# Performance work log

Hardware: AMD Instinct MI355X
Metric: run time of the kernel (lower is better)

The kernel has to match this reference:

```python
import jax, jax.numpy as jnp
import numpy as np

B, S, D, H, HD, FFN_MULT = 4, 2048, 2048, 16, 128, 4
EPS = 1e-8


def setup_inputs() -> dict:
    key = jax.random.key(0)
    ks = jax.random.split(key, 12)
    s = lambda k, shape, scale: (jax.random.normal(k, shape, dtype=jnp.float32) * scale)
    d_ff = D * FFN_MULT
    return {
        "x": s(ks[0], (B, S, D), 1.0),
        # per-head Q/K/V projections, stacked: [H, D, HD] (no bias, as in source)
        "wq": s(ks[1], (H, D, HD), D ** -0.5),
        "wk": s(ks[2], (H, D, HD), D ** -0.5),
        "wv": s(ks[3], (H, D, HD), D ** -0.5),
        # output projection Linear(D, D) with bias
        "wo": s(ks[4], (D, D), D ** -0.5),
        "bo": jnp.zeros((D,), jnp.float32),
        # FFN: Linear(D, d_ff) -> ReLU -> Linear(d_ff, D), both with bias
        "w1": s(ks[5], (D, d_ff), D ** -0.5),
        "b1": jnp.zeros((d_ff,), jnp.float32),
        "w2": s(ks[6], (d_ff, D), d_ff ** -0.5),
        "b2": jnp.zeros((D,), jnp.float32),
        # RMSNorm gains
        "g1": jnp.ones((D,), jnp.float32),
        "g2": jnp.ones((D,), jnp.float32),
    }


def rms_norm(x, g):
    return x * jax.lax.rsqrt(jnp.mean(x * x, axis=-1, keepdims=True) + EPS) * g


def attention(h, wq, wk, wv, wo, bo):
    # per-head projections batched over heads: [B,S,D] x [H,D,K] -> [B,H,S,K]
    q = jnp.einsum("bsd,hdk->bhsk", h, wq)
    k = jnp.einsum("bsd,hdk->bhsk", h, wk)
    v = jnp.einsum("bsd,hdk->bhsk", h, wv)
    scores = jnp.einsum("bhsk,bhtk->bhst", q, k) * (HD ** -0.5)
    causal = jnp.tril(jnp.ones((S, S), dtype=bool))
    scores = jnp.where(causal, scores, -jnp.inf)
    attn = jax.nn.softmax(scores, axis=-1)
    out = jnp.einsum("bhst,bhtk->bhsk", attn, v)  # [B,H,S,HD]
    # concat heads along feature dim (head order matches torch.cat over heads)
    out = out.transpose(0, 2, 1, 3).reshape(B, S, D)
    return out @ wo + bo


def reference(x, wq, wk, wv, wo, bo, w1, b1, w2, b2, g1, g2):
    x = x + attention(rms_norm(x, g1), wq, wk, wv, wo, bo)
    h = rms_norm(x, g2)
    ffn = jax.nn.relu(h @ w1 + b1) @ w2 + b2
    return x + ffn
```

## Files before the change

kernel.cpp:

```cpp
#include <hip/hip_runtime.h>
#include <hip/hip_bf16.h>

#define Bsz 4
#define Ssz 2048
#define Dsz 2048
#define Hn 16
#define HDsz 128
#define DFF 8192
#define Msz (Bsz*Ssz)

typedef __bf16 bf16x8 __attribute__((ext_vector_type(8)));
typedef float  f32x4  __attribute__((ext_vector_type(4)));

enum { FLAG_BIAS=1, FLAG_RELU=2, FLAG_RESID=4, FLAG_F32OUT=8 };

#define GLDS16(g, l) __builtin_amdgcn_global_load_lds( \
    (const __attribute__((address_space(1))) unsigned int*)(g), \
    (__attribute__((address_space(3))) unsigned int*)(l), 16, 0, 0)

template <typename TIN>
__global__ __launch_bounds__(256) void transpose_cvt(
    const TIN* __restrict__ in, __bf16* __restrict__ out,
    int R, int C, long long inRS, int subB,
    long long strideOuter, long long strideInner, long long outBS)
{
  __shared__ float tile[32][33];
  int bz = blockIdx.z;
  const TIN* inp = in + (size_t)(bz / subB) * strideOuter + (size_t)(bz % subB) * strideInner;
  __bf16* outp = out + (size_t)bz * outBS;
  int tx = threadIdx.x, ty = threadIdx.y;
  int c  = blockIdx.x * 32 + tx;
  int r0 = blockIdx.y * 32;
#pragma unroll
  for (int i = 0; i < 4; ++i) {
    int r = r0 + ty + i * 8;
    tile[ty + i * 8][tx] = (float)inp[(size_t)r * inRS + c];
  }
  __syncthreads();
  int oc  = r0 + tx;
  int or0 = blockIdx.x * 32;
#pragma unroll
  for (int i = 0; i < 4; ++i) {
    int orr = or0 + ty + i * 8;
    outp[(size_t)orr * R + oc] = (__bf16)tile[tx][ty + i * 8];
  }
}

__global__ __launch_bounds__(256) void rmsnorm_k(
    const float* __restrict__ x, const float* __restrict__ g, __bf16* __restrict__ out)
{
  int row = blockIdx.x, tid = threadIdx.x;
  const float4* xr = (const float4*)(x + (size_t)row * Dsz);
  float4 v0 = xr[tid*2], v1 = xr[tid*2+1];
  float ss = v0.x*v0.x + v0.y*v0.y + v0.z*v0.z + v0.w*v0.w
           + v1.x*v1.x + v1.y*v1.y + v1.z*v1.z + v1.w*v1.w;
#pragma unroll
  for (int off = 32; off > 0; off >>= 1) ss += __shfl_down(ss, off);
  __shared__ float wsum[4];
  __shared__ float sc;
  if ((tid & 63) == 0) wsum[tid >> 6] = ss;
  __syncthreads();
  if (tid == 0) {
    float t = wsum[0] + wsum[1] + wsum[2] + wsum[3];
    sc = rsqrtf(t * (1.0f / (float)Dsz) + 1e-8f);
  }
  __syncthreads();
  float s = sc;
  const float4* gr = (const float4*)g;
  float4 g0 = gr[tid*2], g1v = gr[tid*2+1];
  bf16x8 ov;
  ov[0]=(__bf16)(v0.x*s*g0.x);  ov[1]=(__bf16)(v0.y*s*g0.y);
  ov[2]=(__bf16)(v0.z*s*g0.z);  ov[3]=(__bf16)(v0.w*s*g0.w);
  ov[4]=(__bf16)(v1.x*s*g1v.x); ov[5]=(__bf16)(v1.y*s*g1v.y);
  ov[6]=(__bf16)(v1.z*s*g1v.z); ov[7]=(__bf16)(v1.w*s*g1v.w);
  *(bf16x8*)(out + (size_t)row * Dsz + tid * 8) = ov;
}

#define SBAR       asm volatile("s_barrier" ::: "memory")
#define WAIT_LGKM0 do { asm volatile("s_waitcnt lgkmcnt(0)" ::: "memory"); \
                        __builtin_amdgcn_sched_barrier(0); } while(0)
#define WAIT_VM4   asm volatile("s_waitcnt vmcnt(4)" ::: "memory")
#define WAIT_VM0   asm volatile("s_waitcnt vmcnt(0)" ::: "memory")

#define STAGE(Xb, Xlds, nb, kh, kst) do { \
    GLDS16((Xb) + (size_t)(rloc      ) * K + (kst) + (kh)*32 + sloc, (Xlds) + (nb)*32768 + (kh)*16384 +        wuni); \
    GLDS16((Xb) + (size_t)(rloc + 128) * K + (kst) + (kh)*32 + sloc, (Xlds) + (nb)*32768 + (kh)*16384 + 8192 + wuni); \
  } while (0)

#define LDA(mh, kh, i) (*(const bf16x8*)(AsB + cur*32768 + (kh)*16384 + (wr*128 + (mh)*64 + (i)*16 + l15)*64 + psl))
#define LDB(kh, j)     (*(const bf16x8*)(BsB + cur*32768 + (kh)*16384 + (wc*64  + (j)*16 + l15)*64 + psl))

#define MFMA16(mh) do { \
  _Pragma("unroll") \
  for (int mi = 0; mi < 4; ++mi) \
    _Pragma("unroll") \
    for (int nj = 0; nj < 4; ++nj) \
      acc[(mh)*4+mi][nj] = __builtin_amdgcn_mfma_f32_16x16x32_bf16(af[mi], bf[nj], acc[(mh)*4+mi][nj], 0, 0, 0); \
} while (0)

__global__ __launch_bounds__(512) void gemm256(
    const __bf16* __restrict__ A, const __bf16* __restrict__ B,
    const float* __restrict__ bias, const float* __restrict__ resid,
    void* __restrict__ Cout, int M, int N, int K, int flags)
{
  __shared__ __align__(16) __bf16 As[2*2*256*32];
  __shared__ __align__(16) __bf16 Bs[2*2*256*32];
  int nwg = gridDim.x;
  int id = blockIdx.x;
  id = (id & 7) * (nwg >> 3) + (id >> 3);
  int ntn = N >> 8;
  int tm = id / ntn, tn = id - tm * ntn;
  int tid = threadIdx.x;
  int lane = tid & 63, w = tid >> 6;
  int l15 = lane & 15, lg = lane >> 4;
  int wr = w >> 2, wc = w & 3;
  const __bf16* Ab = A + (size_t)tm * 256 * K;
  const __bf16* Bb = B + (size_t)tn * 256 * K;
  char* AsB = (char*)As;
  char* BsB = (char*)Bs;
  int rloc = w * 16 + (lane >> 2);
  int sloc = ((lane & 3) ^ ((lane >> 2) & 3)) * 8;
  int wuni = w * 1024;
  int psl  = (lg ^ (l15 & 3)) * 16;
  f32x4 zero; zero[0]=0.f; zero[1]=0.f; zero[2]=0.f; zero[3]=0.f;
  f32x4 acc[8][4];
#pragma unroll
  for (int i = 0; i < 8; ++i)
#pragma unroll
    for (int j = 0; j < 4; ++j) acc[i][j] = zero;
  int NT = K >> 6;
  STAGE(Ab, AsB, 0, 0, 0);
  STAGE(Bb, BsB, 0, 0, 0);
  STAGE(Ab, AsB, 0, 1, 0);
  STAGE(Bb, BsB, 0, 1, 0);
  WAIT_VM4; SBAR;
  int cur = 0;
  for (int t = 0; t < NT; ++t) {
    int nb = cur ^ 1;
    int kst = (t + 1 < NT) ? ((t + 1) << 6) : 0;
    bf16x8 af[4], bf[4];
    STAGE(Ab, AsB, nb, 0, kst);
    af[0]=LDA(0,0,0); af[1]=LDA(0,0,1); af[2]=LDA(0,0,2); af[3]=LDA(0,0,3);
    bf[0]=LDB(0,0);   bf[1]=LDB(0,1);   bf[2]=LDB(0,2);   bf[3]=LDB(0,3);
    SBAR; WAIT_LGKM0;
    __builtin_amdgcn_s_setprio(1); MFMA16(0); __builtin_amdgcn_s_setprio(0);
    SBAR;
    STAGE(Bb, BsB, nb, 0, kst);
    af[0]=LDA(1,0,0); af[1]=LDA(1,0,1); af[2]=LDA(1,0,2); af[3]=LDA(1,0,3);
    SBAR; WAIT_LGKM0;
    __builtin_amdgcn_s_setprio(1); MFMA16(1); __builtin_amdgcn_s_setprio(0);
    WAIT_VM4;
    SBAR;
    STAGE(Ab, AsB, nb, 1, kst);
    af[0]=LDA(0,1,0); af[1]=LDA(0,1,1); af[2]=LDA(0,1,2); af[3]=LDA(0,1,3);
    bf[0]=LDB(1,0);   bf[1]=LDB(1,1);   bf[2]=LDB(1,2);   bf[3]=LDB(1,3);
    SBAR; WAIT_LGKM0;
    __builtin_amdgcn_s_setprio(1); MFMA16(0); __builtin_amdgcn_s_setprio(0);
    SBAR;
    STAGE(Bb, BsB, nb, 1, kst);
    af[0]=LDA(1,1,0); af[1]=LDA(1,1,1); af[2]=LDA(1,1,2); af[3]=LDA(1,1,3);
    SBAR; WAIT_LGKM0;
    __builtin_amdgcn_s_setprio(1); MFMA16(1); __builtin_amdgcn_s_setprio(0);
    WAIT_VM4;
    SBAR;
    cur = nb;
  }
  WAIT_VM0;
  int cm = tm * 256 + wr * 128;
  int cn = tn * 256 + wc * 64;
  float*  Cf = (float*)Cout;
  __bf16* Cb = (__bf16*)Cout;
#pragma unroll
  for (int m = 0; m < 8; ++m) {
#pragma unroll
    for (int nj = 0; nj < 4; ++nj) {
      int col = cn + nj * 16 + l15;
      float bv = (flags & FLAG_BIAS) ? bias[col] : 0.0f;
#pragma unroll
      for (int r = 0; r < 4; ++r) {
        int row = cm + m * 16 + 4 * lg + r;
        float v = acc[m][nj][r] + bv;
        if (flags & FLAG_RELU) v = v > 0.f ? v : 0.f;
        size_t idx = (size_t)row * N + col;
        if (flags & FLAG_RESID) v += resid[idx];
        if (flags & FLAG_F32OUT) Cf[idx] = v;
        else                     Cb[idx] = (__bf16)v;
      }
    }
  }
}

__global__ __launch_bounds__(512) void fattn(
    const __bf16* __restrict__ q, const __bf16* __restrict__ k,
    const __bf16* __restrict__ vt, __bf16* __restrict__ o)
{
  __shared__ __align__(16) __bf16 Ks[64*128];
  __shared__ __align__(16) __bf16 Vs[128*64];
  __shared__ __align__(16) __bf16 Ps[8][16*80];
  int bx = blockIdx.x, bh = blockIdx.y;
  int b = bh >> 4, h = bh & 15;
  int tid = threadIdx.x, lane = tid & 63, w = tid >> 6;
  int l15 = lane & 15, lg = lane >> 4;
  size_t base = ((size_t)b * Ssz) * Dsz + (size_t)h * HDsz;
  size_t vtb  = (size_t)bh * HDsz * Ssz;
  const float scale = 0.08838834764831845f;
  char* KsB = (char*)Ks;
  char* VsB = (char*)Vs;
  f32x4 zero; zero[0]=0.f; zero[1]=0.f; zero[2]=0.f; zero[3]=0.f;

  for (int ph = 0; ph < 2; ++ph) {
    int qt = ph ? bx : (15 - bx);
    int qs = qt * 128;
    int qmin = qs + w * 16;
    bf16x8 qf[4];
    int qrow = qmin + l15;
#pragma unroll
    for (int kk = 0; kk < 4; ++kk)
      qf[kk] = *(const bf16x8*)(q + base + (size_t)qrow * Dsz + kk * 32 + lg * 8);
    f32x4 acc[8];
#pragma unroll
    for (int i = 0; i < 8; ++i) acc[i] = zero;
    float mr[4], lr[4];
#pragma unroll
    for (int r = 0; r < 4; ++r) { mr[r] = -1e30f; lr[r] = 0.f; }
    int NT = 2 * qt + 2;
    for (int kt = 0; kt < NT; ++kt) {
      int t0 = kt * 64;
#pragma unroll
      for (int j = 0; j < 2; ++j) {
        int c = tid + j * 512;
        int tr = c >> 4, hc = c & 15;
        bf16x8 tk = *(const bf16x8*)(k + base + (size_t)(t0 + tr) * Dsz + hc * 8);
        *(bf16x8*)(KsB + ((tr * 256 + hc * 16) ^ ((tr & 7) << 4))) = tk;
        int hd = c >> 3, tc = c & 7;
        bf16x8 tv = *(const bf16x8*)(vt + vtb + (size_t)hd * Ssz + t0 + tc * 8);
        *(bf16x8*)(VsB + ((hd * 128 + tc * 16) ^ ((hd & 7) << 4))) = tv;
      }
      __syncthreads();
      bool act = (t0 <= qmin + 15);
      if (act) {
        f32x4 s[4];
#pragma unroll
        for (int cg = 0; cg < 4; ++cg) s[cg] = zero;
#pragma unroll
        for (int kk = 0; kk < 4; ++kk) {
#pragma unroll
          for (int cg = 0; cg < 4; ++cg) {
            int tl = cg * 16 + l15;
            bf16x8 kf = *(const bf16x8*)(KsB + ((tl * 256 + kk * 64 + lg * 16) ^ ((tl & 7) << 4)));
            s[cg] = __builtin_amdgcn_mfma_f32_16x16x32_bf16(qf[kk], kf, s[cg], 0, 0, 0);
          }
        }
        bool nm = (t0 + 63 > qmin);
        float pv[4][4];
        float al[4];
#pragma unroll
        for (int r = 0; r < 4; ++r) {
          int qr = qmin + 4 * lg + r;
          float rm = -1e30f;
#pragma unroll
          for (int cg = 0; cg < 4; ++cg) {
            float sv = s[cg][r] * scale;
            if (nm && (t0 + cg * 16 + l15) > qr) sv = -1e30f;
            s[cg][r] = sv;
            rm = fmaxf(rm, sv);
          }
          rm = fmaxf(rm, __shfl_xor(rm, 1));
          rm = fmaxf(rm, __shfl_xor(rm, 2));
          rm = fmaxf(rm, __shfl_xor(rm, 4));
          rm = fmaxf(rm, __shfl_xor(rm, 8));
          float mn = fmaxf(mr[r], rm);
          float a = __expf(mr[r] - mn);
          mr[r] = mn;
          float ps = 0.f;
#pragma unroll
          for (int cg = 0; cg < 4; ++cg) {
            float p = __expf(s[cg][r] - mn);
            pv[cg][r] = p;
            ps += p;
          }
          ps += __shfl_xor(ps, 1);
          ps += __shfl_xor(ps, 2);
          ps += __shfl_xor(ps, 4);
          ps += __shfl_xor(ps, 8);
          lr[r] = lr[r] * a + ps;
          al[r] = a;
        }
        f32x4 av; av[0]=al[0]; av[1]=al[1]; av[2]=al[2]; av[3]=al[3];
#pragma unroll
        for (int hg = 0; hg < 8; ++hg) acc[hg] *= av;
#pragma unroll
        for (int cg = 0; cg < 4; ++cg)
#pragma unroll
          for (int r = 0; r < 4; ++r)
            Ps[w][(4 * lg + r) * 80 + cg * 16 + l15] = (__bf16)pv[cg][r];
#pragma unroll
        for (int tt = 0; tt < 2; ++tt) {
          bf16x8 pf = *(const bf16x8*)(&Ps[w][l15 * 80 + tt * 32 + lg * 8]);
#pragma unroll
          for (int hg = 0; hg < 8; ++hg) {
            int hd = hg * 16 + l15;
            bf16x8 vf = *(const bf16x8*)(VsB + ((hd * 128 + tt * 64 + lg * 16) ^ ((hd & 7) << 4)));
            acc[hg] = __builtin_amdgcn_mfma_f32_16x16x32_bf16(pf, vf, acc[hg], 0, 0, 0);
          }
        }
      }
      __syncthreads();
    }
    f32x4 inv;
#pragma unroll
    for (int r = 0; r < 4; ++r) inv[r] = 1.0f / lr[r];
#pragma unroll
    for (int hg = 0; hg < 8; ++hg) {
      f32x4 ov = acc[hg] * inv;
#pragma unroll
      for (int r = 0; r < 4; ++r) {
        int qr2 = qmin + 4 * lg + r;
        o[base + (size_t)qr2 * Dsz + hg * 16 + l15] = (__bf16)ov[r];
      }
    }
  }
}

extern "C" void kernel_launch(void* const* d_in, const int* in_sizes, int n_in,
                              void* d_out, int out_size, void* d_ws, size_t ws_size,
                              hipStream_t stream)
{
  (void)in_sizes; (void)n_in; (void)out_size; (void)ws_size;
  const float* x  = (const float*)d_in[0];
  const float* wq = (const float*)d_in[1];
  const float* wk = (const float*)d_in[2];
  const float* wv = (const float*)d_in[3];
  const float* wo = (const float*)d_in[4];
  const float* bo = (const float*)d_in[5];
  const float* w1 = (const float*)d_in[6];
  const float* b1 = (const float*)d_in[7];
  const float* w2 = (const float*)d_in[8];
  const float* b2 = (const float*)d_in[9];
  const float* g1 = (const float*)d_in[10];
  const float* g2 = (const float*)d_in[11];
  float* out = (float*)d_out;
  char* ws = (char*)d_ws;

  const size_t U = (size_t)2048 * 2048 * 2;
  __bf16* wqT = (__bf16*)(ws);
  __bf16* wkT = (__bf16*)(ws + U);
  __bf16* wvT = (__bf16*)(ws + 2*U);
  __bf16* woT = (__bf16*)(ws + 3*U);
  __bf16* w1T = (__bf16*)(ws + 4*U);
  __bf16* w2T = (__bf16*)(ws + 8*U);
  __bf16* h1  = (__bf16*)(ws + 12*U);
  __bf16* vb  = (__bf16*)(ws + 16*U);
  __bf16* vT    = h1;
  __bf16* attno = vb;
  __bf16* fb    = h1;
  __bf16* h2    = (__bf16*)(ws);
  __bf16* qb = (__bf16*)d_out;
  __bf16* kb = qb + (size_t)Msz * Dsz;
  float*  x2 = (float*)d_out;

  dim3 tb(32, 8, 1);
  transpose_cvt<float><<<dim3(4,64,16),  tb, 0, stream>>>(wq, wqT, 2048, 128, 128, 1, (long long)2048*128, 0, (long long)128*2048);
  transpose_cvt<float><<<dim3(4,64,16),  tb, 0, stream>>>(wk, wkT, 2048, 128, 128, 1, (long long)2048*128, 0, (long long)128*2048);
  transpose_cvt<float><<<dim3(4,64,16),  tb, 0, stream>>>(wv, wvT, 2048, 128, 128, 1, (long long)2048*128, 0, (long long)128*2048);
  transpose_cvt<float><<<dim3(64,64,1),  tb, 0, stream>>>(wo, woT, 2048, 2048, 2048, 1, 0, 0, 0);
  transpose_cvt<float><<<dim3(256,64,1), tb, 0, stream>>>(w1, w1T, 2048, 8192, 8192, 1, 0, 0, 0);
  transpose_cvt<float><<<dim3(64,128,2), tb, 0, stream>>>(w2, w2T, 4096, 2048, 2048, 1, (long long)4096*2048, 0, (long long)2048*4096);
  rmsnorm_k<<<8192, 256, 0, stream>>>(x, g1, h1);
  gemm256<<<256, 512, 0, stream>>>(h1, wqT, nullptr, nullptr, qb, Msz, 2048, 2048, 0);
  gemm256<<<256, 512, 0, stream>>>(h1, wkT, nullptr, nullptr, kb, Msz, 2048, 2048, 0);
  gemm256<<<256, 512, 0, stream>>>(h1, wvT, nullptr, nullptr, vb, Msz, 2048, 2048, 0);
  transpose_cvt<__bf16><<<dim3(4,64,64), tb, 0, stream>>>(vb, vT, 2048, 128, 2048, 16, (long long)2048*2048, 128, (long long)128*2048);
  fattn<<<dim3(8, 64), 512, 0, stream>>>(qb, kb, vT, attno);
  gemm256<<<256, 512, 0, stream>>>(attno, woT, bo, x, x2, Msz, 2048, 2048, FLAG_BIAS | FLAG_RESID | FLAG_F32OUT);
  rmsnorm_k<<<8192, 256, 0, stream>>>(x2, g2, h2);
  for (int c = 0; c < 2; ++c) {
    gemm256<<<512, 512, 0, stream>>>(h2, w1T + (size_t)c*4096*2048, b1 + c*4096, nullptr,
                                     fb, Msz, 4096, 2048, FLAG_BIAS | FLAG_RELU);
    int fl = FLAG_RESID | FLAG_F32OUT | (c == 0 ? FLAG_BIAS : 0);
    gemm256<<<256, 512, 0, stream>>>(fb, w2T + (size_t)c*2048*4096, b2, x2,
                                     out, Msz, 2048, 4096, fl);
  }
}
```

Measured before the change: 1.525 ms.

## Deepen GEMM pipeline to four-stage ring of 32-wide K slices

New measurement: 1.675 ms. +9.9%, slower.

```diff
diff --git a/kernel.cpp b/kernel.cpp
--- a/kernel.cpp
+++ b/kernel.cpp
@@ -79,16 +79,16 @@
 #define SBAR       asm volatile("s_barrier" ::: "memory")
 #define WAIT_LGKM0 do { asm volatile("s_waitcnt lgkmcnt(0)" ::: "memory"); \
                         __builtin_amdgcn_sched_barrier(0); } while(0)
-#define WAIT_VM4   asm volatile("s_waitcnt vmcnt(4)" ::: "memory")
+#define WAIT_VM8   asm volatile("s_waitcnt vmcnt(8)" ::: "memory")
 #define WAIT_VM0   asm volatile("s_waitcnt vmcnt(0)" ::: "memory")
 
-#define STAGE(Xb, Xlds, nb, kh, kst) do { \
-    GLDS16((Xb) + (size_t)(rloc      ) * K + (kst) + (kh)*32 + sloc, (Xlds) + (nb)*32768 + (kh)*16384 +        wuni); \
-    GLDS16((Xb) + (size_t)(rloc + 128) * K + (kst) + (kh)*32 + sloc, (Xlds) + (nb)*32768 + (kh)*16384 + 8192 + wuni); \
+#define STG(Xb, Xlds, buf, kst) do { \
+    GLDS16((Xb) + (size_t)(rloc      ) * K + (kst) + sloc, (Xlds) + (buf)*16384 +        wuni); \
+    GLDS16((Xb) + (size_t)(rloc + 128) * K + (kst) + sloc, (Xlds) + (buf)*16384 + 8192 + wuni); \
   } while (0)
 
-#define LDA(mh, kh, i) (*(const bf16x8*)(AsB + cur*32768 + (kh)*16384 + (wr*128 + (mh)*64 + (i)*16 + l15)*64 + psl))
-#define LDB(kh, j)     (*(const bf16x8*)(BsB + cur*32768 + (kh)*16384 + (wc*64  + (j)*16 + l15)*64 + psl))
+#define LDA(mh, i) (*(const bf16x8*)(AsB + cur*16384 + (wr*128 + (mh)*64 + (i)*16 + l15)*64 + psl))
+#define LDB(j)     (*(const bf16x8*)(BsB + cur*16384 + (wc*64  + (j)*16 + l15)*64 + psl))
 
 #define MFMA16(mh) do { \
   _Pragma("unroll") \
@@ -103,8 +103,8 @@
     const float* __restrict__ bias, const float* __restrict__ resid,
     void* __restrict__ Cout, int M, int N, int K, int flags)
 {
-  __shared__ __align__(16) __bf16 As[2*2*256*32];
-  __shared__ __align__(16) __bf16 Bs[2*2*256*32];
+  __shared__ __align__(16) __bf16 As[4*256*32];
+  __shared__ __align__(16) __bf16 Bs[4*256*32];
   int nwg = gridDim.x;
   int id = blockIdx.x;
   id = (id & 7) * (nwg >> 3) + (id >> 3);
@@ -119,51 +119,36 @@
   char* AsB = (char*)As;
   char* BsB = (char*)Bs;
   int rloc = w * 16 + (lane >> 2);
-  int sloc = ((lane & 3) ^ ((lane >> 2) & 3)) * 8;
+  int sloc = ((lane & 3) ^ ((lane >> 3) & 3)) * 8;
   int wuni = w * 1024;
-  int psl  = (lg ^ (l15 & 3)) * 16;
+  int psl  = (lg ^ ((l15 >> 1) & 3)) * 16;
   f32x4 zero; zero[0]=0.f; zero[1]=0.f; zero[2]=0.f; zero[3]=0.f;
   f32x4 acc[8][4];
 #pragma unroll
   for (int i = 0; i < 8; ++i)
 #pragma unroll
     for (int j = 0; j < 4; ++j) acc[i][j] = zero;
-  int NT = K >> 6;
-  STAGE(Ab, AsB, 0, 0, 0);
-  STAGE(Bb, BsB, 0, 0, 0);
-  STAGE(Ab, AsB, 0, 1, 0);
-  STAGE(Bb, BsB, 0, 1, 0);
-  WAIT_VM4; SBAR;
-  int cur = 0;
+  int NT = K >> 5;
+  STG(Ab, AsB, 0, 0);  STG(Bb, BsB, 0, 0);
+  STG(Ab, AsB, 1, 32); STG(Bb, BsB, 1, 32);
+  STG(Ab, AsB, 2, 64); STG(Bb, BsB, 2, 64);
+  WAIT_VM8; SBAR;
   for (int t = 0; t < NT; ++t) {
-    int nb = cur ^ 1;
-    int kst = (t + 1 < NT) ? ((t + 1) << 6) : 0;
+    int cur = t & 3, sb = (t + 3) & 3;
+    int kst = (t + 3 < NT) ? ((t + 3) << 5) : 0;
     bf16x8 af[4], bf[4];
-    STAGE(Ab, AsB, nb, 0, kst);
-    af[0]=LDA(0,0,0); af[1]=LDA(0,0,1); af[2]=LDA(0,0,2); af[3]=LDA(0,0,3);
-    bf[0]=LDB(0,0);   bf[1]=LDB(0,1);   bf[2]=LDB(0,2);   bf[3]=LDB(0,3);
+    STG(Ab, AsB, sb, kst);
+    af[0]=LDA(0,0); af[1]=LDA(0,1); af[2]=LDA(0,2); af[3]=LDA(0,3);
+    bf[0]=LDB(0);   bf[1]=LDB(1);   bf[2]=LDB(2);   bf[3]=LDB(3);
     SBAR; WAIT_LGKM0;
     __builtin_amdgcn_s_setprio(1); MFMA16(0); __builtin_amdgcn_s_setprio(0);
     SBAR;
-    STAGE(Bb, BsB, nb, 0, kst);
-    af[0]=LDA(1,0,0); af[1]=LDA(1,0,1); af[2]=LDA(1,0,2); af[3]=LDA(1,0,3);
+    STG(Bb, BsB, sb, kst);
+    af[0]=LDA(1,0); af[1]=LDA(1,1); af[2]=LDA(1,2); af[3]=LDA(1,3);
     SBAR; WAIT_LGKM0;
     __builtin_amdgcn_s_setprio(1); MFMA16(1); __builtin_amdgcn_s_setprio(0);
-    WAIT_VM4;
+    WAIT_VM8;
     SBAR;
-    STAGE(Ab, AsB, nb, 1, kst);
-    af[0]=LDA(0,1,0); af[1]=LDA(0,1,1); af[2]=LDA(0,1,2); af[3]=LDA(0,1,3);
-    bf[0]=LDB(1,0);   bf[1]=LDB(1,1);   bf[2]=LDB(1,2);   bf[3]=LDB(1,3);
-    SBAR; WAIT_LGKM0;
-    __builtin_amdgcn_s_setprio(1); MFMA16(0); __builtin_amdgcn_s_setprio(0);
-    SBAR;
-    STAGE(Bb, BsB, nb, 1, kst);
-    af[0]=LDA(1,1,0); af[1]=LDA(1,1,1); af[2]=LDA(1,1,2); af[3]=LDA(1,1,3);
-    SBAR; WAIT_LGKM0;
-    __builtin_amdgcn_s_setprio(1); MFMA16(1); __builtin_amdgcn_s_setprio(0);
-    WAIT_VM4;
-    SBAR;
-    cur = nb;
   }
   WAIT_VM0;
   int cm = tm * 256 + wr * 128;
```
